# Optimization experiments

Measured on AMD Instinct MI355X. Metric: run time of the kernel, lower is better.

Reference implementation:

```python
import jax, jax.numpy as jnp
import numpy as np

P, N, H, W, K = 100000, 8, 256, 256, 8
EPS = 1e-12  # F.normalize clamp_min eps


def setup_inputs() -> dict:
    key = jax.random.key(0)
    ks = jax.random.split(key, 12)
    normals = jax.random.normal(ks[3], (P, 3), jnp.float32)
    normals = normals / jnp.linalg.norm(normals, axis=-1, keepdims=True)
    return {
        "idx": jax.random.randint(ks[0], (N, H, W, K), 0, P),
        "dists": jax.random.uniform(ks[1], (N, H, W, K), dtype=jnp.float32),
        "points": jax.random.normal(ks[2], (P, 3), jnp.float32),
        "normals": normals,
        "light_location": jax.random.normal(ks[4], (1, 3), jnp.float32) * 2.0,
        "light_ambient": jax.random.uniform(ks[5], (1, 3), dtype=jnp.float32),
        "light_diffuse": jax.random.uniform(ks[6], (1, 3), dtype=jnp.float32),
        "light_specular": jax.random.uniform(ks[7], (1, 3), dtype=jnp.float32),
        "mat_ambient": jax.random.uniform(ks[8], (1, 3), dtype=jnp.float32),
        "mat_diffuse": jax.random.uniform(ks[9], (1, 3), dtype=jnp.float32),
        "mat_specular": jax.random.uniform(ks[10], (1, 3), dtype=jnp.float32),
        "camera_position": jax.random.normal(ks[11], (1, 3), jnp.float32) * 3.0,
        "shininess": 64,
    }


def _normalize(v):
    return v / jnp.clip(jnp.linalg.norm(v, axis=-1, keepdims=True), 1e-6)


def reference(idx, dists, points, normals, light_location, light_ambient,
              light_diffuse, light_specular, mat_ambient, mat_diffuse,
              mat_specular, camera_position, shininess):
    # masked gather: invalid (idx < 0) pixels read point 0
    safe_idx = jnp.where(idx < 0, 0, idx)                      # (N,H,W,K)
    pix_pts = points[safe_idx]                                 # (N,H,W,K,3)
    pix_nrm = normals[safe_idx]                                # (N,H,W,K,3)

    # point-light Phong shading (pytorch3d _apply_lighting)
    dir_light = _normalize(light_location - pix_pts)           # (N,H,W,K,3)
    cos = jnp.sum(pix_nrm * dir_light, axis=-1, keepdims=True)  # (N,H,W,K,1)
    diffuse = light_diffuse * jax.nn.relu(cos) * mat_diffuse

    view = _normalize(camera_position - pix_pts)
    reflect = 2.0 * cos * pix_nrm - dir_light
    alpha = jax.nn.relu(jnp.sum(view * reflect, axis=-1)) * (cos[..., 0] > 0)
    specular = light_specular * (alpha ** shininess)[..., None] * mat_specular

    ambient = light_ambient * mat_ambient                      # (1,3) broadcast
    colors = ambient + diffuse + specular                      # (N,H,W,K,3)

    # L1-normalized distance weights over K, weighted sum
    dist_mask = jnp.where(dists != -1.0, dists, 0.0)
    wn = dist_mask / jnp.clip(jnp.sum(jnp.abs(dist_mask), axis=-1, keepdims=True), EPS)
    images = jnp.sum(wn[..., None] * colors, axis=-2)          # (N,H,W,3)
    return images
```

## Files before the change

### kernel.cpp

```cpp
#include <hip/hip_runtime.h>

#define K 8

__global__ __launch_bounds__(256) void shading_compositor_kernel(
    const int*   __restrict__ idx,
    const float* __restrict__ dists,
    const float* __restrict__ points,
    const float* __restrict__ normals,
    const float* __restrict__ light_location,
    const float* __restrict__ light_ambient,
    const float* __restrict__ light_diffuse,
    const float* __restrict__ light_specular,
    const float* __restrict__ mat_ambient,
    const float* __restrict__ mat_diffuse,
    const float* __restrict__ mat_specular,
    const float* __restrict__ camera_position,
    const int*   __restrict__ shininess_p,
    float*       __restrict__ out,
    int n_pix)
{
    const int p = blockIdx.x * blockDim.x + threadIdx.x;
    if (p >= n_pix) return;

    const float Lx = light_location[0], Ly = light_location[1], Lz = light_location[2];
    const float Cx = camera_position[0], Cy = camera_position[1], Cz = camera_position[2];
    const float amb0 = light_ambient[0] * mat_ambient[0];
    const float amb1 = light_ambient[1] * mat_ambient[1];
    const float amb2 = light_ambient[2] * mat_ambient[2];
    const float dif0 = light_diffuse[0] * mat_diffuse[0];
    const float dif1 = light_diffuse[1] * mat_diffuse[1];
    const float dif2 = light_diffuse[2] * mat_diffuse[2];
    const float spc0 = light_specular[0] * mat_specular[0];
    const float spc1 = light_specular[1] * mat_specular[1];
    const float spc2 = light_specular[2] * mat_specular[2];
    const int   shin = shininess_p[0];

    const int4*   idxv  = reinterpret_cast<const int4*>(idx   + (size_t)p * K);
    const float4* dstv  = reinterpret_cast<const float4*>(dists + (size_t)p * K);
    int4   i0 = idxv[0], i1 = idxv[1];
    float4 d0 = dstv[0], d1 = dstv[1];

    int   ik[K] = {i0.x, i0.y, i0.z, i0.w, i1.x, i1.y, i1.z, i1.w};
    float dk[K] = {d0.x, d0.y, d0.z, d0.w, d1.x, d1.y, d1.z, d1.w};

    float w[K];
    float wsum = 0.f;
#pragma unroll
    for (int k = 0; k < K; ++k) {
        float d = dk[k];
        float m = (d != -1.0f) ? d : 0.0f;
        w[k] = m;
        wsum += fabsf(m);
    }
    const float winv = 1.0f / fmaxf(wsum, 1e-12f);

    float acc0 = 0.f, acc1 = 0.f, acc2 = 0.f;

#pragma unroll
    for (int k = 0; k < K; ++k) {
        const int ii = (ik[k] < 0) ? 0 : ik[k];
        const size_t base = (size_t)ii * 3;
        const float px = points[base], py = points[base + 1], pz = points[base + 2];
        const float nx = normals[base], ny = normals[base + 1], nz = normals[base + 2];

        float lx = Lx - px, ly = Ly - py, lz = Lz - pz;
        float ll = lx * lx + ly * ly + lz * lz;
        float li = (ll > 1e-12f) ? rsqrtf(ll) : 1e6f;
        lx *= li; ly *= li; lz *= li;

        const float cosv = nx * lx + ny * ly + nz * lz;

        float vx = Cx - px, vy = Cy - py, vz = Cz - pz;
        float vv = vx * vx + vy * vy + vz * vz;
        float vi = (vv > 1e-12f) ? rsqrtf(vv) : 1e6f;
        vx *= vi; vy *= vi; vz *= vi;

        const float c2 = 2.0f * cosv;
        const float rx = c2 * nx - lx;
        const float ry = c2 * ny - ly;
        const float rz = c2 * nz - lz;

        float alpha = fmaxf(vx * rx + vy * ry + vz * rz, 0.0f);
        if (!(cosv > 0.0f)) alpha = 0.0f;

        float sp = 1.0f, b = alpha;
        int e = shin;
        while (e > 0) {
            if (e & 1) sp *= b;
            b *= b;
            e >>= 1;
        }

        const float rc = fmaxf(cosv, 0.0f);
        const float wn = w[k] * winv;
        acc0 += wn * (amb0 + dif0 * rc + spc0 * sp);
        acc1 += wn * (amb1 + dif1 * rc + spc1 * sp);
        acc2 += wn * (amb2 + dif2 * rc + spc2 * sp);
    }

    float* o = out + (size_t)p * 3;
    o[0] = acc0;
    o[1] = acc1;
    o[2] = acc2;
}

extern "C" void kernel_launch(void* const* d_in, const int* in_sizes, int n_in,
                              void* d_out, int out_size, void* d_ws, size_t ws_size,
                              hipStream_t stream) {
    const int*   idx             = (const int*)d_in[0];
    const float* dists           = (const float*)d_in[1];
    const float* points          = (const float*)d_in[2];
    const float* normals         = (const float*)d_in[3];
    const float* light_location  = (const float*)d_in[4];
    const float* light_ambient   = (const float*)d_in[5];
    const float* light_diffuse   = (const float*)d_in[6];
    const float* light_specular  = (const float*)d_in[7];
    const float* mat_ambient     = (const float*)d_in[8];
    const float* mat_diffuse     = (const float*)d_in[9];
    const float* mat_specular    = (const float*)d_in[10];
    const float* camera_position = (const float*)d_in[11];
    const int*   shininess       = (const int*)d_in[12];
    float*       out             = (float*)d_out;

    const int n_pix = in_sizes[0] / K;
    const int block = 256;
    const int grid  = (n_pix + block - 1) / block;

    shading_compositor_kernel<<<grid, block, 0, stream>>>(
        idx, dists, points, normals, light_location, light_ambient,
        light_diffuse, light_specular, mat_ambient, mat_diffuse,
        mat_specular, camera_position, shininess, out, n_pix);
}
```

Before: 135.4 us.

## Pack points and normals into interleaved float4 records for gather

Adds a pre-pass kernel that repacks points and normals into a workspace as two adjacent float4 records per point. The shading kernel then fetches each gathered point with two 16-byte loads from one 32-byte span, replacing six scalar loads spread over two arrays. The weight normalisation is also moved out of the loop so it is applied once per pixel. The cost is an extra kernel launch and a 3.2 MB write on every call, and the packed path runs only when the workspace is large enough.

After: 124.4 us. 1.09x faster.

```diff
diff --git a/kernel.cpp b/kernel.cpp
--- a/kernel.cpp
+++ b/kernel.cpp
@@ -2,21 +2,42 @@
 
 #define K 8
 
-__global__ __launch_bounds__(256) void shading_compositor_kernel(
-    const int*   __restrict__ idx,
-    const float* __restrict__ dists,
+__global__ __launch_bounds__(256) void pack_pn_kernel(
     const float* __restrict__ points,
     const float* __restrict__ normals,
-    const float* __restrict__ light_location,
-    const float* __restrict__ light_ambient,
-    const float* __restrict__ light_diffuse,
-    const float* __restrict__ light_specular,
-    const float* __restrict__ mat_ambient,
-    const float* __restrict__ mat_diffuse,
-    const float* __restrict__ mat_specular,
-    const float* __restrict__ camera_position,
-    const int*   __restrict__ shininess_p,
-    float*       __restrict__ out,
+    float4*      __restrict__ rec,
+    int P)
+{
+    const int i = blockIdx.x * blockDim.x + threadIdx.x;
+    if (i >= P) return;
+    const size_t b = (size_t)i * 3;
+    rec[2 * i]     = make_float4(points[b],  points[b + 1],  points[b + 2],  0.0f);
+    rec[2 * i + 1] = make_float4(normals[b], normals[b + 1], normals[b + 2], 0.0f);
+}
+
+struct ShadeConsts {
+    float Lx, Ly, Lz, Cx, Cy, Cz;
+    float amb0, amb1, amb2, dif0, dif1, dif2, spc0, spc1, spc2;
+    int shin;
+};
+
+template <bool PACKED>
+__global__ __launch_bounds__(256) void shading_compositor_kernel(
+    const int*    __restrict__ idx,
+    const float*  __restrict__ dists,
+    const float*  __restrict__ points,
+    const float*  __restrict__ normals,
+    const float4* __restrict__ rec,
+    const float*  __restrict__ light_location,
+    const float*  __restrict__ light_ambient,
+    const float*  __restrict__ light_diffuse,
+    const float*  __restrict__ light_specular,
+    const float*  __restrict__ mat_ambient,
+    const float*  __restrict__ mat_diffuse,
+    const float*  __restrict__ mat_specular,
+    const float*  __restrict__ camera_position,
+    const int*    __restrict__ shininess_p,
+    float*        __restrict__ out,
     int n_pix)
 {
     const int p = blockIdx.x * blockDim.x + threadIdx.x;
@@ -35,8 +56,8 @@
     const float spc2 = light_specular[2] * mat_specular[2];
     const int   shin = shininess_p[0];
 
-    const int4*   idxv  = reinterpret_cast<const int4*>(idx   + (size_t)p * K);
-    const float4* dstv  = reinterpret_cast<const float4*>(dists + (size_t)p * K);
+    const int4*   idxv = reinterpret_cast<const int4*>(idx   + (size_t)p * K);
+    const float4* dstv = reinterpret_cast<const float4*>(dists + (size_t)p * K);
     int4   i0 = idxv[0], i1 = idxv[1];
     float4 d0 = dstv[0], d1 = dstv[1];
 
@@ -59,9 +80,17 @@
 #pragma unroll
     for (int k = 0; k < K; ++k) {
         const int ii = (ik[k] < 0) ? 0 : ik[k];
-        const size_t base = (size_t)ii * 3;
-        const float px = points[base], py = points[base + 1], pz = points[base + 2];
-        const float nx = normals[base], ny = normals[base + 1], nz = normals[base + 2];
+        float px, py, pz, nx, ny, nz;
+        if (PACKED) {
+            const float4 pr = rec[2 * (size_t)ii];
+            const float4 nr = rec[2 * (size_t)ii + 1];
+            px = pr.x; py = pr.y; pz = pr.z;
+            nx = nr.x; ny = nr.y; nz = nr.z;
+        } else {
+            const size_t base = (size_t)ii * 3;
+            px = points[base];  py = points[base + 1];  pz = points[base + 2];
+            nx = normals[base]; ny = normals[base + 1]; nz = normals[base + 2];
+        }
 
         float lx = Lx - px, ly = Ly - py, lz = Lz - pz;
         float ll = lx * lx + ly * ly + lz * lz;
@@ -92,16 +121,16 @@
         }
 
         const float rc = fmaxf(cosv, 0.0f);
-        const float wn = w[k] * winv;
-        acc0 += wn * (amb0 + dif0 * rc + spc0 * sp);
-        acc1 += wn * (amb1 + dif1 * rc + spc1 * sp);
-        acc2 += wn * (amb2 + dif2 * rc + spc2 * sp);
+        const float wk = w[k];
+        acc0 += wk * (amb0 + dif0 * rc + spc0 * sp);
+        acc1 += wk * (amb1 + dif1 * rc + spc1 * sp);
+        acc2 += wk * (amb2 + dif2 * rc + spc2 * sp);
     }
 
     float* o = out + (size_t)p * 3;
-    o[0] = acc0;
-    o[1] = acc1;
-    o[2] = acc2;
+    o[0] = acc0 * winv;
+    o[1] = acc1 * winv;
+    o[2] = acc2 * winv;
 }
 
 extern "C" void kernel_launch(void* const* d_in, const int* in_sizes, int n_in,
@@ -123,11 +152,23 @@
     float*       out             = (float*)d_out;
 
     const int n_pix = in_sizes[0] / K;
+    const int P     = in_sizes[2] / 3;
+
     const int block = 256;
     const int grid  = (n_pix + block - 1) / block;
 
-    shading_compositor_kernel<<<grid, block, 0, stream>>>(
-        idx, dists, points, normals, light_location, light_ambient,
-        light_diffuse, light_specular, mat_ambient, mat_diffuse,
-        mat_specular, camera_position, shininess, out, n_pix);
+    const size_t need = (size_t)P * 2 * sizeof(float4);
+    if (ws_size >= need) {
+        float4* rec = (float4*)d_ws;
+        pack_pn_kernel<<<(P + block - 1) / block, block, 0, stream>>>(points, normals, rec, P);
+        shading_compositor_kernel<true><<<grid, block, 0, stream>>>(
+            idx, dists, points, normals, rec, light_location, light_ambient,
+            light_diffuse, light_specular, mat_ambient, mat_diffuse,
+            mat_specular, camera_position, shininess, out, n_pix);
+    } else {
+        shading_compositor_kernel<false><<<grid, block, 0, stream>>>(
+            idx, dists, points, normals, nullptr, light_location, light_ambient,
+            light_diffuse, light_specular, mat_ambient, mat_diffuse,
+            mat_specular, camera_position, shininess, out, n_pix);
+    }
 }
```
